# Optimization experiments

Measured on AMD Instinct MI355X. Metric: run time of the kernel, lower is better.

## Reference

```python
import jax, jax.numpy as jnp
import numpy as np

CH = 256
IC = 128  # inter_channels = channels // reduction
TEMP = 0.05


def setup_inputs() -> dict:
    key = jax.random.key(0)
    k1, k2, k3, k4, k5 = jax.random.split(key, 5)
    x = jax.random.normal(k1, (8, CH, 64, 64), dtype=jnp.float32)
    # 1x1 conv weights stored as [out_ch, in_ch]
    w_qkv = jax.random.normal(k2, (3 * IC, CH), dtype=jnp.float32) * 0.01
    b_qkv = jax.random.normal(k3, (3 * IC,), dtype=jnp.float32) * 0.01
    w_out = jax.random.normal(k4, (CH, IC), dtype=jnp.float32) * 0.01
    b_out = jax.random.normal(k5, (CH,), dtype=jnp.float32) * 0.01
    return {"x": x, "w_qkv": w_qkv, "b_qkv": b_qkv, "w_out": w_out, "b_out": b_out}


def reference(x, w_qkv, b_qkv, w_out, b_out):
    b, c, h, w = x.shape
    n = h * w
    ic = w_qkv.shape[0] // 3
    # 1x1 conv QKV projection
    qkv = jnp.einsum('bchw,oc->bohw', x, w_qkv) + b_qkv[None, :, None, None]
    qkv = qkv.reshape(b, 3, ic, n)
    q, k, v = qkv[:, 0], qkv[:, 1], qkv[:, 2]  # each [b, ic, n]
    # mean-center q and k over spatial positions (per channel)
    k = k - k.mean(axis=-1, keepdims=True)
    q = q - q.mean(axis=-1, keepdims=True)
    # pairwise_weight[b, i, j] = sum_c k[b, c, i] * q[b, c, j]
    pw = jnp.einsum('bci,bcj->bij', k, q)
    pw = pw / jnp.sqrt(jnp.float32(ic))  # use_scale=True
    pw = pw / TEMP
    pw = jax.nn.softmax(pw, axis=-1)  # [b, n, n]
    # y[b, c, i] = sum_j pw[b, i, j] * v[b, c, j]
    y = jnp.einsum('bij,bcj->bci', pw, v).reshape(b, ic, h, w)
    out = x + jnp.einsum('bchw,oc->bohw', y, w_out) + b_out[None, :, None, None]
    return out
```

## Files before the change

### kernel.cpp

```cpp
#include <hip/hip_runtime.h>
#include <hip/hip_bf16.h>

typedef __bf16 bf16_t;
typedef __bf16 bf16x8 __attribute__((ext_vector_type(8)));
typedef float f32x4 __attribute__((ext_vector_type(4)));
typedef float f32x16 __attribute__((ext_vector_type(16)));

#define MFMA16(a, b, c) __builtin_amdgcn_mfma_f32_16x16x32_bf16((a), (b), (c), 0, 0, 0)
#define MFMA32(a, b, c) __builtin_amdgcn_mfma_f32_32x32x16_bf16((a), (b), (c), 0, 0, 0)

constexpr int CH = 256, IC = 128, NPOS = 4096;
constexpr float SM_C = 2.5503488f;

constexpr size_t OFF_XT    = 0;
constexpr size_t OFF_QT    = 16777216;
constexpr size_t OFF_KT    = 25165824;
constexpr size_t OFF_V     = 33554432;
constexpr size_t OFF_WQKV  = 41943040;
constexpr size_t OFF_WOUT  = 42139648;
constexpr size_t OFF_QKM   = 42213376;
constexpr size_t OFF_PL    = 42221568;

__device__ __forceinline__ void gload_lds16(const char* g, char* lds) {
    __builtin_amdgcn_global_load_lds((const __attribute__((address_space(1))) unsigned int*)g,
                                     (__attribute__((address_space(3))) unsigned int*)lds, 16, 0,
                                     0);
}
__device__ __forceinline__ float fexp2(float x) {
    float r;
    asm("v_exp_f32 %0, %1" : "=v"(r) : "v"(x));
    return r;
}
__device__ __forceinline__ int cvtpk(float lo, float hi) {
    int r;
    asm("v_cvt_pk_bf16_f32 %0, %1, %2" : "=v"(r) : "v"(lo), "v"(hi));
    return r;
}

__global__ void k_prep1(const float* __restrict__ x, const float* __restrict__ wqkv,
                        const float* __restrict__ wout, bf16_t* __restrict__ xt,
                        float* __restrict__ xpart, bf16_t* __restrict__ wqkv_b,
                        bf16_t* __restrict__ wout_b) {
    int bid = blockIdx.x;
    if (bid >= 8192) {
        int idx = (bid - 8192) * 256 + threadIdx.x;
        if (idx < 384 * 256) wqkv_b[idx] = (bf16_t)wqkv[idx];
        int j = idx - 384 * 256;
        if (j >= 0 && j < 256 * 128) wout_b[j] = (bf16_t)wout[j];
        return;
    }
    __shared__ float t[32][33];
    int p0 = (bid & 127) * 32, c0 = ((bid >> 7) & 7) * 32, b = bid >> 10;
    int i = threadIdx.x >> 5, j = threadIdx.x & 31;
#pragma unroll
    for (int q = 0; q < 4; q++) {
        int c = c0 + q * 8 + i;
        t[q * 8 + i][j] = x[((size_t)(b * CH + c)) * NPOS + p0 + j];
    }
    __syncthreads();
#pragma unroll
    for (int q = 0; q < 4; q++) {
        int p = p0 + q * 8 + i;
        xt[((size_t)(b * NPOS + p)) * CH + c0 + j] = (bf16_t)t[j][q * 8 + i];
    }
    int cl = threadIdx.x >> 3, part = threadIdx.x & 7;
    float s = 0.f;
#pragma unroll
    for (int u = 0; u < 4; u++) s += t[cl][part * 4 + u];
    s += __shfl_down(s, 4, 64);
    s += __shfl_down(s, 2, 64);
    s += __shfl_down(s, 1, 64);
    if (part == 0) xpart[((size_t)(b * 128) + (p0 >> 5)) * 256 + c0 + cl] = s;
}

__global__ void k_small(const float* __restrict__ xpart, const float* __restrict__ wqkv,
                        float* __restrict__ qkm) {
    int b = blockIdx.x, t = threadIdx.x;
    __shared__ float xm[256];
    float s = 0.f;
    const float* xp = xpart + (size_t)(b * 128) * 256 + t;
#pragma unroll 8
    for (int i = 0; i < 128; i++) s += xp[i * 256];
    xm[t] = s * (1.0f / NPOS);
    __syncthreads();
    float acc = 0.f;
    const float4* w = (const float4*)(wqkv + (size_t)t * CH);
#pragma unroll
    for (int c4 = 0; c4 < 64; c4++) {
        float4 w4 = w[c4];
        acc += w4.x * xm[c4 * 4] + w4.y * xm[c4 * 4 + 1] + w4.z * xm[c4 * 4 + 2] +
               w4.w * xm[c4 * 4 + 3];
    }
    qkm[b * CH + t] = acc;
}

__global__ __launch_bounds__(256, 2) void k_qkv(const bf16_t* __restrict__ xt,
                                                const bf16_t* __restrict__ wqkv_b,
                                                const float* __restrict__ qkm,
                                                const float* __restrict__ b_qkv,
                                                bf16_t* __restrict__ qt, bf16_t* __restrict__ kt,
                                                bf16_t* __restrict__ v) {
    int bid = blockIdx.x;
    int b = bid & 7;
    int r0 = bid >> 3;
    int sec = r0 % 3;
    int pt = r0 / 3;
    int p0 = pt * 128;
    int wid = threadIdx.x >> 6, lane = threadIdx.x & 63;
    int g = lane >> 4, li = lane & 15;
    int wr = wid >> 1, wc = wid & 1;
    f32x4 acc[4][4] = {};
    if (sec < 2) {
        int ob = sec * 128;
#pragma unroll 1
        for (int kk = 0; kk < 8; kk++) {
            bf16x8 af[4], bfg[4];
#pragma unroll
            for (int fa = 0; fa < 4; fa++) {
                int p = p0 + wr * 64 + fa * 16 + li;
                af[fa] = *(const bf16x8*)(xt + ((size_t)(b * NPOS + p)) * CH + kk * 32 + g * 8);
            }
#pragma unroll
            for (int fb = 0; fb < 4; fb++) {
                int o = ob + wc * 64 + fb * 16 + li;
                bfg[fb] = *(const bf16x8*)(wqkv_b + (size_t)o * CH + kk * 32 + g * 8);
            }
#pragma unroll
            for (int fa = 0; fa < 4; fa++)
#pragma unroll
                for (int fb = 0; fb < 4; fb++) acc[fa][fb] = MFMA16(af[fa], bfg[fb], acc[fa][fb]);
        }
        bf16_t* dst = (sec == 0) ? qt : kt;
        float scale = (sec == 1) ? SM_C : 1.0f;
#pragma unroll
        for (int fb = 0; fb < 4; fb++) {
            int ol = wc * 64 + fb * 16 + li;
            float mean = qkm[b * CH + sec * 128 + ol];
#pragma unroll
            for (int fa = 0; fa < 4; fa++)
#pragma unroll
                for (int r = 0; r < 4; r++) {
                    int p = p0 + wr * 64 + fa * 16 + g * 4 + r;
                    dst[((size_t)(b * NPOS + p)) * IC + ol] =
                        (bf16_t)((acc[fa][fb][r] - mean) * scale);
                }
        }
    } else {
#pragma unroll 1
        for (int kk = 0; kk < 8; kk++) {
            bf16x8 af[4], bfg[4];
#pragma unroll
            for (int fa = 0; fa < 4; fa++) {
                int o = 256 + wr * 64 + fa * 16 + li;
                af[fa] = *(const bf16x8*)(wqkv_b + (size_t)o * CH + kk * 32 + g * 8);
            }
#pragma unroll
            for (int fb = 0; fb < 4; fb++) {
                int p = p0 + wc * 64 + fb * 16 + li;
                bfg[fb] = *(const bf16x8*)(xt + ((size_t)(b * NPOS + p)) * CH + kk * 32 + g * 8);
            }
#pragma unroll
            for (int fa = 0; fa < 4; fa++)
#pragma unroll
                for (int fb = 0; fb < 4; fb++) acc[fa][fb] = MFMA16(af[fa], bfg[fb], acc[fa][fb]);
        }
#pragma unroll
        for (int fa = 0; fa < 4; fa++)
#pragma unroll
            for (int r = 0; r < 4; r++) {
                int oe = wr * 64 + fa * 16 + g * 4 + r;
                float bias = b_qkv[256 + oe];
#pragma unroll
                for (int fb = 0; fb < 4; fb++) {
                    int p = p0 + wc * 64 + fb * 16 + li;
                    v[((size_t)(b * IC + oe)) * NPOS + p] = (bf16_t)(acc[fa][fb][r] + bias);
                }
            }
    }
}

constexpr int TJ = 64;

__global__ __launch_bounds__(512, 1) void k_attn(const bf16_t* __restrict__ qt,
                                                 const bf16_t* __restrict__ kt,
                                                 const bf16_t* __restrict__ v,
                                                 bf16_t* __restrict__ pacc,
                                                 float* __restrict__ pl) {
    __shared__ __attribute__((aligned(128))) char smem[2 * 32768];
    const int bid = blockIdx.x;
    const int b = bid & 7;
    const int jh = (bid >> 3) & 1;
    const int it = bid >> 4;
    const int jbase = jh * 2048;
    const int t = threadIdx.x;
    const int wid = t >> 6, lane = t & 63;
    const int col = lane & 31, h = lane >> 5;
    const int jw = wid & 1, ih = wid >> 1;
    const int iw0 = it * 128 + ih * 32;
    const bf16_t* ktb = kt + (size_t)b * NPOS * IC;
    const bf16_t* qtb = qt + (size_t)b * NPOS * IC;
    const bf16_t* vb = v + (size_t)b * IC * NPOS;

    int qoff_[2], voff_[2];
#pragma unroll
    for (int u = 0; u < 2; u++) {
        int row = u * 32 + (t >> 4);
        qoff_[u] = row * 256 + (((t & 15) ^ (row & 15)) << 4);
        int src = (t & 15) ^ (row & 15);
        voff_[u] = (row + (src >> 3) * 64) * 8192 + (src & 7) * 16;
    }

    auto stage = [&](int dstpar, int sj) {
        const char* qs = (const char*)qtb + (size_t)sj * 256;
        const char* vs = (const char*)vb + (size_t)sj * 2;
        char* qd = smem + dstpar * 32768;
        char* vd = qd + 16384;
#pragma unroll
        for (int u = 0; u < 2; u++) {
            gload_lds16(qs + qoff_[u], qd + u * 8192 + t * 16);
            gload_lds16(vs + voff_[u], vd + u * 8192 + t * 16);
        }
    };

    bf16x8 bk[8];
#pragma unroll
    for (int ks = 0; ks < 8; ks++)
        bk[ks] = *(const bf16x8*)(ktb + (size_t)(iw0 + col) * IC + ks * 16 + h * 8);

    stage(0, jbase);

    f32x16 acc[4] = {};
    float ls[4] = {0.f, 0.f, 0.f, 0.f};

    auto body = [&](int par, int nextj) {
        stage(par ^ 1, nextj);
        asm volatile("s_waitcnt vmcnt(4)" ::: "memory");
        __builtin_amdgcn_s_barrier();
        asm volatile("" ::: "memory");
        const char* qb = smem + par * 32768;
        const char* vbuf = qb + 16384;
        f32x16 s = {};
        __builtin_amdgcn_s_setprio(1);
#pragma unroll
        for (int ks = 0; ks < 8; ks++) {
            bf16x8 aq = *(const bf16x8*)(qb + (jw * 32 + col) * 256 +
                                         (((ks * 2 + h) ^ (col & 15)) << 4));
            s = MFMA32(aq, bk[ks], s);
        }
        __builtin_amdgcn_s_setprio(0);
        float e[16];
#pragma unroll
        for (int r = 0; r < 16; r++) e[r] = fexp2(s[r]);
#pragma unroll
        for (int r = 0; r < 16; r++) ls[r & 3] += e[r];
        int w[8];
#pragma unroll
        for (int q = 0; q < 8; q++) w[q] = cvtpk(e[2 * q], e[2 * q + 1]);
        asm("v_permlane32_swap_b32 %0, %1" : "+v"(w[0]), "+v"(w[2]));
        asm("v_permlane32_swap_b32 %0, %1" : "+v"(w[1]), "+v"(w[3]));
        asm("v_permlane32_swap_b32 %0, %1" : "+v"(w[4]), "+v"(w[6]));
        asm("v_permlane32_swap_b32 %0, %1" : "+v"(w[5]), "+v"(w[7]));
        union {
            int u[4];
            bf16x8 v;
        } pb0, pb1;
        pb0.u[0] = w[0]; pb0.u[1] = w[1]; pb0.u[2] = w[2]; pb0.u[3] = w[3];
        pb1.u[0] = w[4]; pb1.u[1] = w[5]; pb1.u[2] = w[6]; pb1.u[3] = w[7];
        __builtin_amdgcn_s_setprio(1);
#pragma unroll
        for (int kl = 0; kl < 2; kl++) {
            int kg = jw * 2 + kl;
            bf16x8 pbf = kl == 0 ? pb0.v : pb1.v;
#pragma unroll
            for (int cs = 0; cs < 4; cs++) {
                int crow = (cs & 1) * 32 + col;
                int p = ((cs >> 1) * 8 + kg * 2 + h) ^ (crow & 15);
                bf16x8 av = *(const bf16x8*)(vbuf + crow * 256 + (p << 4));
                acc[cs] = MFMA32(av, pbf, acc[cs]);
            }
        }
        __builtin_amdgcn_s_setprio(0);
        asm volatile("" ::: "memory");
        __builtin_amdgcn_s_barrier();
    };

#pragma unroll 1
    for (int jo = 0; jo < 2048; jo += 2 * TJ) {
        body(0, jbase + ((jo + TJ) & 2047));
        body(1, jbase + ((jo + 2 * TJ) & 2047));
    }

    asm volatile("s_waitcnt vmcnt(0)" ::: "memory");
    __syncthreads();
    float* rb = (float*)smem;
    float lsum = (ls[0] + ls[1]) + (ls[2] + ls[3]);
    if (jw == 1) {
        float* db = rb + ih * 4096;
#pragma unroll
        for (int cs = 0; cs < 4; cs++)
#pragma unroll
            for (int q = 0; q < 4; q++) {
                f32x4 tv = {acc[cs][4 * q], acc[cs][4 * q + 1], acc[cs][4 * q + 2],
                            acc[cs][4 * q + 3]};
                *(f32x4*)(db + (cs * 4 + q) * 256 + lane * 4) = tv;
            }
    }
    __syncthreads();
    if (jw == 0) {
        const float* db = rb + ih * 4096;
#pragma unroll
        for (int cs = 0; cs < 4; cs++)
#pragma unroll
            for (int q = 0; q < 4; q++) {
                f32x4 r = *(const f32x4*)(db + (cs * 4 + q) * 256 + lane * 4);
#pragma unroll
                for (int e2 = 0; e2 < 4; e2++) acc[cs][4 * q + e2] += r[e2];
            }
    }
    __syncthreads();
    if (jw == 1) rb[ih * 64 + lane] = lsum;
    __syncthreads();
    if (jw == 0) {
        lsum += rb[ih * 64 + lane];
        lsum += __shfl_xor(lsum, 32, 64);
        const int i = iw0 + col;
        if (h == 0) pl[((size_t)(b * 2 + jh)) * NPOS + i] = lsum;
        bf16_t* po = pacc + ((size_t)(b * 2 + jh)) * NPOS * IC;
#pragma unroll
        for (int cs = 0; cs < 4; cs++)
#pragma unroll
            for (int q = 0; q < 8; q++) {
                int u = cvtpk(acc[cs][2 * q], acc[cs][2 * q + 1]);
                int c0 = cs * 32 + ((q & 1) << 1) + ((q >> 1) << 3) + 4 * h;
                *(int*)((char*)po + ((size_t)i * IC + c0) * 2) = u;
            }
    }
}

__global__ __launch_bounds__(256, 2) void k_out(const bf16_t* __restrict__ pacc,
                                                const float* __restrict__ pl,
                                                const bf16_t* __restrict__ wout_b,
                                                const float* __restrict__ x,
                                                const float* __restrict__ b_out,
                                                float* __restrict__ out) {
    int bid = blockIdx.x;
    int b = bid & 7;
    int r0 = bid >> 3;
    int oct = r0 & 1, pt = r0 >> 1;
    int p0 = pt * 128, oc0 = oct * 128;
    int wid = threadIdx.x >> 6, lane = threadIdx.x & 63;
    int g = lane >> 4, li = lane & 15;
    int wr = wid >> 1, wc = wid & 1;
    const bf16_t* pa0 = pacc + (size_t)(b * 2 + 0) * NPOS * IC;
    const bf16_t* pa1 = pacc + (size_t)(b * 2 + 1) * NPOS * IC;
    float inv[4];
#pragma unroll
    for (int fb = 0; fb < 4; fb++) {
        int p = p0 + wc * 64 + fb * 16 + li;
        inv[fb] = 1.0f / (pl[(size_t)(b * 2 + 0) * NPOS + p] + pl[(size_t)(b * 2 + 1) * NPOS + p]);
    }
    f32x4 acc[4][4] = {};
#pragma unroll
    for (int kk = 0; kk < 4; kk++) {
        bf16x8 af[4], bfg[4];
#pragma unroll
        for (int fa = 0; fa < 4; fa++) {
            int oc = oc0 + wr * 64 + fa * 16 + li;
            af[fa] = *(const bf16x8*)(wout_b + (size_t)oc * IC + kk * 32 + g * 8);
        }
#pragma unroll
        for (int fb = 0; fb < 4; fb++) {
            int p = p0 + wc * 64 + fb * 16 + li;
            bf16x8 a0 = *(const bf16x8*)(pa0 + (size_t)p * IC + kk * 32 + g * 8);
            bf16x8 a1 = *(const bf16x8*)(pa1 + (size_t)p * IC + kk * 32 + g * 8);
#pragma unroll
            for (int e = 0; e < 8; e++)
                bfg[fb][e] = (bf16_t)(((float)a0[e] + (float)a1[e]) * inv[fb]);
        }
#pragma unroll
        for (int fa = 0; fa < 4; fa++)
#pragma unroll
            for (int fb = 0; fb < 4; fb++) acc[fa][fb] = MFMA16(af[fa], bfg[fb], acc[fa][fb]);
    }
#pragma unroll
    for (int fa = 0; fa < 4; fa++)
#pragma unroll
        for (int r = 0; r < 4; r++) {
            int oc = oc0 + wr * 64 + fa * 16 + g * 4 + r;
            float bias = b_out[oc];
#pragma unroll
            for (int fb = 0; fb < 4; fb++) {
                int p = p0 + wc * 64 + fb * 16 + li;
                size_t idx = ((size_t)(b * CH + oc)) * NPOS + p;
                out[idx] = acc[fa][fb][r] + x[idx] + bias;
            }
        }
}

extern "C" void kernel_launch(void* const* d_in, const int* in_sizes, int n_in, void* d_out,
                              int out_size, void* d_ws, size_t ws_size, hipStream_t stream) {
    const float* x = (const float*)d_in[0];
    const float* w_qkv = (const float*)d_in[1];
    const float* b_qkv = (const float*)d_in[2];
    const float* w_out = (const float*)d_in[3];
    const float* b_out = (const float*)d_in[4];
    float* out = (float*)d_out;
    char* ws = (char*)d_ws;

    bf16_t* xt = (bf16_t*)(ws + OFF_XT);
    bf16_t* pacc = (bf16_t*)(ws + OFF_XT);
    bf16_t* qt = (bf16_t*)(ws + OFF_QT);
    bf16_t* kt = (bf16_t*)(ws + OFF_KT);
    bf16_t* v = (bf16_t*)(ws + OFF_V);
    float* xpart = (float*)(ws + OFF_V);
    bf16_t* wqkv_b = (bf16_t*)(ws + OFF_WQKV);
    bf16_t* wout_b = (bf16_t*)(ws + OFF_WOUT);
    float* qkm = (float*)(ws + OFF_QKM);
    float* pl = (float*)(ws + OFF_PL);

    k_prep1<<<8704, 256, 0, stream>>>(x, w_qkv, w_out, xt, xpart, wqkv_b, wout_b);
    k_small<<<8, 256, 0, stream>>>(xpart, w_qkv, qkm);
    k_qkv<<<768, 256, 0, stream>>>(xt, wqkv_b, qkm, b_qkv, qt, kt, v);
    k_attn<<<512, 512, 0, stream>>>(qt, kt, v, pacc, pl);
    k_out<<<512, 256, 0, stream>>>(pacc, pl, wout_b, x, b_out, out);
}
```

Baseline: 156.0 us.

## Double per-wave query-row tile in attention kernel to reuse staged Q/V tiles

Each wave now handles two 32-row i-tiles (64 rows), so a block covers 256 rows and the grid drops from 512 to 256 blocks. Every Q and V fragment read from LDS feeds two MFMAs instead of one, halving LDS staging and global traffic per unit of work. The cost is double the accumulator and K registers per wave. With 256 blocks on a 256-CU MI355X there is one block per CU and no spare blocks to balance load.

After: 213.5 us. 36.9% more time.

```diff
diff --git a/kernel.cpp b/kernel.cpp
--- a/kernel.cpp
+++ b/kernel.cpp
@@ -195,8 +195,8 @@
     const int t = threadIdx.x;
     const int wid = t >> 6, lane = t & 63;
     const int col = lane & 31, h = lane >> 5;
-    const int jw = wid & 1, ih = wid >> 1;
-    const int iw0 = it * 128 + ih * 32;
+    const int jw = wid & 1, iw = wid >> 1;
+    const int iw0 = it * 256 + iw * 64;
     const bf16_t* ktb = kt + (size_t)b * NPOS * IC;
     const bf16_t* qtb = qt + (size_t)b * NPOS * IC;
     const bf16_t* vb = v + (size_t)b * IC * NPOS;
@@ -222,37 +222,24 @@
         }
     };
 
-    bf16x8 bk[8];
-#pragma unroll
-    for (int ks = 0; ks < 8; ks++)
-        bk[ks] = *(const bf16x8*)(ktb + (size_t)(iw0 + col) * IC + ks * 16 + h * 8);
+    bf16x8 bk0[8], bk1[8];
+#pragma unroll
+    for (int ks = 0; ks < 8; ks++) {
+        bk0[ks] = *(const bf16x8*)(ktb + (size_t)(iw0 + col) * IC + ks * 16 + h * 8);
+        bk1[ks] = *(const bf16x8*)(ktb + (size_t)(iw0 + 32 + col) * IC + ks * 16 + h * 8);
+    }
 
     stage(0, jbase);
 
-    f32x16 acc[4] = {};
-    float ls[4] = {0.f, 0.f, 0.f, 0.f};
-
-    auto body = [&](int par, int nextj) {
-        stage(par ^ 1, nextj);
-        asm volatile("s_waitcnt vmcnt(4)" ::: "memory");
-        __builtin_amdgcn_s_barrier();
-        asm volatile("" ::: "memory");
-        const char* qb = smem + par * 32768;
-        const char* vbuf = qb + 16384;
-        f32x16 s = {};
-        __builtin_amdgcn_s_setprio(1);
-#pragma unroll
-        for (int ks = 0; ks < 8; ks++) {
-            bf16x8 aq = *(const bf16x8*)(qb + (jw * 32 + col) * 256 +
-                                         (((ks * 2 + h) ^ (col & 15)) << 4));
-            s = MFMA32(aq, bk[ks], s);
-        }
-        __builtin_amdgcn_s_setprio(0);
+    f32x16 acc0[4] = {}, acc1[4] = {};
+    float ls0[4] = {}, ls1[4] = {};
+
+    auto packP = [&](const f32x16& s, float* lsx, bf16x8& o0, bf16x8& o1) {
         float e[16];
 #pragma unroll
         for (int r = 0; r < 16; r++) e[r] = fexp2(s[r]);
 #pragma unroll
-        for (int r = 0; r < 16; r++) ls[r & 3] += e[r];
+        for (int r = 0; r < 16; r++) lsx[r & 3] += e[r];
         int w[8];
 #pragma unroll
         for (int q = 0; q < 8; q++) w[q] = cvtpk(e[2 * q], e[2 * q + 1]);
@@ -263,20 +250,46 @@
         union {
             int u[4];
             bf16x8 v;
-        } pb0, pb1;
-        pb0.u[0] = w[0]; pb0.u[1] = w[1]; pb0.u[2] = w[2]; pb0.u[3] = w[3];
-        pb1.u[0] = w[4]; pb1.u[1] = w[5]; pb1.u[2] = w[6]; pb1.u[3] = w[7];
+        } t0, t1;
+        t0.u[0] = w[0]; t0.u[1] = w[1]; t0.u[2] = w[2]; t0.u[3] = w[3];
+        t1.u[0] = w[4]; t1.u[1] = w[5]; t1.u[2] = w[6]; t1.u[3] = w[7];
+        o0 = t0.v;
+        o1 = t1.v;
+    };
+
+    auto body = [&](int par, int nextj) {
+        stage(par ^ 1, nextj);
+        asm volatile("s_waitcnt vmcnt(4)" ::: "memory");
+        __builtin_amdgcn_s_barrier();
+        asm volatile("" ::: "memory");
+        const char* qb = smem + par * 32768;
+        const char* vbuf = qb + 16384;
+        f32x16 sA = {}, sB = {};
+        __builtin_amdgcn_s_setprio(1);
+#pragma unroll
+        for (int ks = 0; ks < 8; ks++) {
+            bf16x8 aq = *(const bf16x8*)(qb + (jw * 32 + col) * 256 +
+                                         (((ks * 2 + h) ^ (col & 15)) << 4));
+            sA = MFMA32(aq, bk0[ks], sA);
+            sB = MFMA32(aq, bk1[ks], sB);
+        }
+        __builtin_amdgcn_s_setprio(0);
+        bf16x8 pA0, pA1, pB0, pB1;
+        packP(sA, ls0, pA0, pA1);
+        packP(sB, ls1, pB0, pB1);
         __builtin_amdgcn_s_setprio(1);
 #pragma unroll
         for (int kl = 0; kl < 2; kl++) {
             int kg = jw * 2 + kl;
-            bf16x8 pbf = kl == 0 ? pb0.v : pb1.v;
+            bf16x8 pA = kl ? pA1 : pA0;
+            bf16x8 pB = kl ? pB1 : pB0;
 #pragma unroll
             for (int cs = 0; cs < 4; cs++) {
                 int crow = (cs & 1) * 32 + col;
                 int p = ((cs >> 1) * 8 + kg * 2 + h) ^ (crow & 15);
                 bf16x8 av = *(const bf16x8*)(vbuf + crow * 256 + (p << 4));
-                acc[cs] = MFMA32(av, pbf, acc[cs]);
+                acc0[cs] = MFMA32(av, pA, acc0[cs]);
+                acc1[cs] = MFMA32(av, pB, acc1[cs]);
             }
         }
         __builtin_amdgcn_s_setprio(0);
@@ -293,47 +306,85 @@
     asm volatile("s_waitcnt vmcnt(0)" ::: "memory");
     __syncthreads();
     float* rb = (float*)smem;
-    float lsum = (ls[0] + ls[1]) + (ls[2] + ls[3]);
+    float lsA = (ls0[0] + ls0[1]) + (ls0[2] + ls0[3]);
+    float lsB = (ls1[0] + ls1[1]) + (ls1[2] + ls1[3]);
     if (jw == 1) {
-        float* db = rb + ih * 4096;
+        float* db = rb + iw * 4096;
 #pragma unroll
         for (int cs = 0; cs < 4; cs++)
 #pragma unroll
             for (int q = 0; q < 4; q++) {
-                f32x4 tv = {acc[cs][4 * q], acc[cs][4 * q + 1], acc[cs][4 * q + 2],
-                            acc[cs][4 * q + 3]};
+                f32x4 tv = {acc0[cs][4 * q], acc0[cs][4 * q + 1], acc0[cs][4 * q + 2],
+                            acc0[cs][4 * q + 3]};
                 *(f32x4*)(db + (cs * 4 + q) * 256 + lane * 4) = tv;
             }
     }
     __syncthreads();
     if (jw == 0) {
-        const float* db = rb + ih * 4096;
+        const float* db = rb + iw * 4096;
 #pragma unroll
         for (int cs = 0; cs < 4; cs++)
 #pragma unroll
             for (int q = 0; q < 4; q++) {
                 f32x4 r = *(const f32x4*)(db + (cs * 4 + q) * 256 + lane * 4);
 #pragma unroll
-                for (int e2 = 0; e2 < 4; e2++) acc[cs][4 * q + e2] += r[e2];
-            }
-    }
-    __syncthreads();
-    if (jw == 1) rb[ih * 64 + lane] = lsum;
+                for (int e2 = 0; e2 < 4; e2++) acc0[cs][4 * q + e2] += r[e2];
+            }
+    }
+    __syncthreads();
+    if (jw == 1) {
+        float* db = rb + iw * 4096;
+#pragma unroll
+        for (int cs = 0; cs < 4; cs++)
+#pragma unroll
+            for (int q = 0; q < 4; q++) {
+                f32x4 tv = {acc1[cs][4 * q], acc1[cs][4 * q + 1], acc1[cs][4 * q + 2],
+                            acc1[cs][4 * q + 3]};
+                *(f32x4*)(db + (cs * 4 + q) * 256 + lane * 4) = tv;
+            }
+    }
     __syncthreads();
     if (jw == 0) {
-        lsum += rb[ih * 64 + lane];
-        lsum += __shfl_xor(lsum, 32, 64);
-        const int i = iw0 + col;
-        if (h == 0) pl[((size_t)(b * 2 + jh)) * NPOS + i] = lsum;
+        const float* db = rb + iw * 4096;
+#pragma unroll
+        for (int cs = 0; cs < 4; cs++)
+#pragma unroll
+            for (int q = 0; q < 4; q++) {
+                f32x4 r = *(const f32x4*)(db + (cs * 4 + q) * 256 + lane * 4);
+#pragma unroll
+                for (int e2 = 0; e2 < 4; e2++) acc1[cs][4 * q + e2] += r[e2];
+            }
+    }
+    __syncthreads();
+    if (jw == 1) {
+        rb[(iw * 2 + 0) * 64 + lane] = lsA;
+        rb[(iw * 2 + 1) * 64 + lane] = lsB;
+    }
+    __syncthreads();
+    if (jw == 0) {
+        lsA += rb[(iw * 2 + 0) * 64 + lane];
+        lsB += rb[(iw * 2 + 1) * 64 + lane];
+        lsA += __shfl_xor(lsA, 32, 64);
+        lsB += __shfl_xor(lsB, 32, 64);
+        if (h == 0) {
+            pl[((size_t)(b * 2 + jh)) * NPOS + iw0 + col] = lsA;
+            pl[((size_t)(b * 2 + jh)) * NPOS + iw0 + 32 + col] = lsB;
+        }
         bf16_t* po = pacc + ((size_t)(b * 2 + jh)) * NPOS * IC;
 #pragma unroll
-        for (int cs = 0; cs < 4; cs++)
-#pragma unroll
-            for (int q = 0; q < 8; q++) {
-                int u = cvtpk(acc[cs][2 * q], acc[cs][2 * q + 1]);
-                int c0 = cs * 32 + ((q & 1) << 1) + ((q >> 1) << 3) + 4 * h;
-                *(int*)((char*)po + ((size_t)i * IC + c0) * 2) = u;
-            }
+        for (int it2 = 0; it2 < 2; it2++) {
+            int i = iw0 + it2 * 32 + col;
+#pragma unroll
+            for (int cs = 0; cs < 4; cs++) {
+                const f32x16& A = it2 ? acc1[cs] : acc0[cs];
+#pragma unroll
+                for (int q = 0; q < 8; q++) {
+                    int u = cvtpk(A[2 * q], A[2 * q + 1]);
+                    int c0 = cs * 32 + ((q & 1) << 1) + ((q >> 1) << 3) + 4 * h;
+                    *(int*)((char*)po + ((size_t)i * IC + c0) * 2) = u;
+                }
+            }
+        }
     }
 }
 
@@ -421,6 +472,6 @@
     k_prep1<<<8704, 256, 0, stream>>>(x, w_qkv, w_out, xt, xpart, wqkv_b, wout_b);
     k_small<<<8, 256, 0, stream>>>(xpart, w_qkv, qkm);
     k_qkv<<<768, 256, 0, stream>>>(xt, wqkv_b, qkm, b_qkv, qt, kt, v);
-    k_attn<<<512, 512, 0, stream>>>(qt, kt, v, pacc, pl);
+    k_attn<<<256, 512, 0, stream>>>(qt, kt, v, pacc, pl);
     k_out<<<512, 256, 0, stream>>>(pacc, pl, wout_b, x, b_out, out);
 }
```
